# Optimization experiments

Hardware: AMD Instinct MI355X
Metric: run time of the kernel (lower is better)

Reference implementation:

```python
import jax, jax.numpy as jnp
import numpy as np

NUM_FIELDS = 39
PER_FIELD_VOCAB = 10000
TOTAL_VOCAB = NUM_FIELDS * PER_FIELD_VOCAB
EMBED_DIM = 128
DIM_INT = (2, 3)
RANKS = (128, 128)
BATCH = 2048


def setup_inputs() -> dict:
    key = jax.random.key(0)
    k_x, k_emb, k_lin, k_b, k_w0, k_w1 = jax.random.split(key, 6)
    x = jax.random.randint(k_x, (BATCH, NUM_FIELDS), 0, PER_FIELD_VOCAB, dtype=jnp.int64 if jax.config.jax_enable_x64 else jnp.int32)
    embed_table = jax.random.normal(k_emb, (TOTAL_VOCAB, EMBED_DIM), dtype=jnp.float32) * 0.01
    linear_table = jax.random.normal(k_lin, (TOTAL_VOCAB, 1), dtype=jnp.float32) * 0.01
    bias = jnp.zeros((1,), dtype=jnp.float32)
    # trunc_normal_(std=0.01) approximated by scaled normal (same distribution family)
    W0 = jax.random.normal(k_w0, (DIM_INT[0], RANKS[0], NUM_FIELDS), dtype=jnp.float32) * 0.01
    W1 = jax.random.normal(k_w1, (DIM_INT[1], RANKS[1], NUM_FIELDS), dtype=jnp.float32) * 0.01
    return {"x": x, "embed_table": embed_table, "linear_table": linear_table,
            "bias": bias, "W0": W0, "W1": W1}


def _calc_cross(emb, W):
    # emb: [B, F, D]; W: [L, R, F]
    # dot_products[b,d,r,l] = sum_f W[l,r,f] * emb[b,f,d]   (torch: 'bljk,bki->bijl')
    dp = jnp.einsum('lrf,bfd->bdrl', W, emb)          # [B, D, R, L]
    prod_over_l = jnp.prod(dp, axis=3)                # [B, D, R]
    return jnp.sum(prod_over_l, axis=(1, 2))[:, None]  # [B, 1]


def reference(x, embed_table, linear_table, bias, W0, W1):
    # per-field offsets into the flat embedding table (FeaturesEmbedding behavior)
    offsets = (jnp.arange(NUM_FIELDS) * PER_FIELD_VOCAB).astype(x.dtype)
    idx = x + offsets[None, :]                        # [B, F]
    emb = embed_table[idx]                            # [B, F, D]
    # FeaturesLinear: sum of per-feature weights + bias -> [B, 1]
    ret = jnp.sum(linear_table[idx], axis=1) + bias
    for W in (W0, W1):
        ret = ret + _calc_cross(emb, W)
    return (ret, 0)
```

## Files before the change

kernel.cpp:

```cpp
#include <hip/hip_runtime.h>
#include <hip/hip_bf16.h>

#define NUM_FIELDS 39
#define PER_FIELD_VOCAB 10000
#define EMBED_DIM 128
#define KPAD 64
#define NL 5
#define RANK 128
#define BATCH 2048
#define LDS_STRIDE 72

typedef __bf16  bf16x8  __attribute__((ext_vector_type(8)));
typedef float   f32x4   __attribute__((ext_vector_type(4)));

__global__ __launch_bounds__(256) void prep_w(const float* __restrict__ W0,
                                              const float* __restrict__ W1,
                                              __bf16* __restrict__ Wb) {
    int i = blockIdx.x * 256 + threadIdx.x;
    if (i >= NL * RANK * KPAD) return;
    int f = i & (KPAD - 1);
    int r = (i >> 6) & (RANK - 1);
    int l = i >> 13;
    float v = 0.f;
    if (f < NUM_FIELDS) {
        if (l < 2) v = W0[(l * RANK + r) * NUM_FIELDS + f];
        else       v = W1[((l - 2) * RANK + r) * NUM_FIELDS + f];
    }
    Wb[i] = (__bf16)v;
}

__global__ __launch_bounds__(256) void tfm_main(const int* __restrict__ x,
                                                const float* __restrict__ embed_table,
                                                const float* __restrict__ linear_table,
                                                const float* __restrict__ bias,
                                                const __bf16* __restrict__ Wb,
                                                float* __restrict__ out,
                                                int out_size) {
    __shared__ int   sidx[NUM_FIELDS];
    __shared__ __align__(16) __bf16 eT[EMBED_DIM * LDS_STRIDE];
    __shared__ float wpart[4];

    const int tid = threadIdx.x;
    const int b   = blockIdx.x;

    if (tid < NUM_FIELDS)
        sidx[tid] = x[b * NUM_FIELDS + tid] + tid * PER_FIELD_VOCAB;
    __syncthreads();

    for (int k = tid; k < NUM_FIELDS * EMBED_DIM; k += 256) {
        int f = k >> 7, d = k & (EMBED_DIM - 1);
        float v = embed_table[(long)sidx[f] * EMBED_DIM + d];
        eT[d * LDS_STRIDE + f] = (__bf16)v;
    }
    for (int k = tid; k < (KPAD - NUM_FIELDS) * EMBED_DIM; k += 256) {
        int f = NUM_FIELDS + (k >> 7), d = k & (EMBED_DIM - 1);
        eT[d * LDS_STRIDE + f] = (__bf16)0.f;
    }

    float partial = 0.f;
    if (tid < NUM_FIELDS) partial = linear_table[sidx[tid]];

    __syncthreads();

    const int wave = tid >> 6, lane = tid & 63;
    const int m = lane & 15, quad = lane >> 4;

    for (int rti = 0; rti < 2; ++rti) {
        const int r0 = (wave * 2 + rti) * 16;
        bf16x8 afrag[NL][2];
#pragma unroll
        for (int l = 0; l < NL; ++l)
#pragma unroll
            for (int kc = 0; kc < 2; ++kc)
                afrag[l][kc] = *reinterpret_cast<const bf16x8*>(
                    &Wb[((size_t)(l * RANK) + r0 + m) * KPAD + kc * 32 + quad * 8]);

        for (int dt = 0; dt < 8; ++dt) {
            const int d0 = dt * 16;
            bf16x8 bfrag[2];
#pragma unroll
            for (int kc = 0; kc < 2; ++kc)
                bfrag[kc] = *reinterpret_cast<const bf16x8*>(
                    &eT[(d0 + m) * LDS_STRIDE + kc * 32 + quad * 8]);

            f32x4 acc[NL];
#pragma unroll
            for (int l = 0; l < NL; ++l) {
                acc[l] = (f32x4){0.f, 0.f, 0.f, 0.f};
#pragma unroll
                for (int kc = 0; kc < 2; ++kc)
                    acc[l] = __builtin_amdgcn_mfma_f32_16x16x32_bf16(
                        afrag[l][kc], bfrag[kc], acc[l], 0, 0, 0);
            }
#pragma unroll
            for (int i = 0; i < 4; ++i)
                partial += acc[0][i] * acc[1][i] + acc[2][i] * acc[3][i] * acc[4][i];
        }
    }

#pragma unroll
    for (int off = 32; off > 0; off >>= 1)
        partial += __shfl_down(partial, off, 64);
    if (lane == 0) wpart[wave] = partial;
    __syncthreads();
    if (tid == 0)
        out[b] = wpart[0] + wpart[1] + wpart[2] + wpart[3] + bias[0];

    if (b == 0)
        for (int j = BATCH + tid; j < out_size; j += 256)
            out[j] = 0.f;
}

extern "C" void kernel_launch(void* const* d_in, const int* in_sizes, int n_in,
                              void* d_out, int out_size, void* d_ws, size_t ws_size,
                              hipStream_t stream) {
    const int*   x            = (const int*)d_in[0];
    const float* embed_table  = (const float*)d_in[1];
    const float* linear_table = (const float*)d_in[2];
    const float* bias         = (const float*)d_in[3];
    const float* W0           = (const float*)d_in[4];
    const float* W1           = (const float*)d_in[5];
    __bf16*      Wb           = (__bf16*)d_ws;

    prep_w<<<(NL * RANK * KPAD + 255) / 256, 256, 0, stream>>>(W0, W1, Wb);
    tfm_main<<<BATCH, 256, 0, stream>>>(x, embed_table, linear_table, bias, Wb,
                                        (float*)d_out, out_size);
}
```

Baseline: 278.1 us.

## Switch to 32x32x16 MFMA tiles with K padded to 48 and hoisted weight loads

Replaces the 16x16x32 MFMA tiling with 32x32x16 tiles, so each wave handles 32 ranks across all 128 embedding dims. The reduction dimension is padded to 48 instead of 64, which cuts the wasted MFMA work on zero fields. Weight fragments are loaded before the embedding gather so their latency overlaps it. The gather now writes four fields per packed LDS store, with zero padding built in, removing the separate zero-fill loop. The cost is more accumulator registers (five 16-float accumulators plus psum), which may lower occupancy.

```diff
diff --git a/kernel.cpp b/kernel.cpp
--- a/kernel.cpp
+++ b/kernel.cpp
@@ -4,23 +4,25 @@
 #define NUM_FIELDS 39
 #define PER_FIELD_VOCAB 10000
 #define EMBED_DIM 128
-#define KPAD 64
+#define KPAD 48
 #define NL 5
 #define RANK 128
 #define BATCH 2048
-#define LDS_STRIDE 72
+#define LDE 56
 
 typedef __bf16  bf16x8  __attribute__((ext_vector_type(8)));
-typedef float   f32x4   __attribute__((ext_vector_type(4)));
+typedef __bf16  bf16x4  __attribute__((ext_vector_type(4)));
+typedef float   f32x16  __attribute__((ext_vector_type(16)));
 
 __global__ __launch_bounds__(256) void prep_w(const float* __restrict__ W0,
                                               const float* __restrict__ W1,
                                               __bf16* __restrict__ Wb) {
     int i = blockIdx.x * 256 + threadIdx.x;
     if (i >= NL * RANK * KPAD) return;
-    int f = i & (KPAD - 1);
-    int r = (i >> 6) & (RANK - 1);
-    int l = i >> 13;
+    int f  = i % KPAD;
+    int rl = i / KPAD;
+    int r  = rl & (RANK - 1);
+    int l  = rl >> 7;
     float v = 0.f;
     if (f < NUM_FIELDS) {
         if (l < 2) v = W0[(l * RANK + r) * NUM_FIELDS + f];
@@ -37,66 +39,79 @@
                                                 float* __restrict__ out,
                                                 int out_size) {
     __shared__ int   sidx[NUM_FIELDS];
-    __shared__ __align__(16) __bf16 eT[EMBED_DIM * LDS_STRIDE];
+    __shared__ __align__(16) __bf16 eT[EMBED_DIM * LDE];
     __shared__ float wpart[4];
 
-    const int tid = threadIdx.x;
-    const int b   = blockIdx.x;
+    const int tid  = threadIdx.x;
+    const int b    = blockIdx.x;
+    const int wave = tid >> 6, lane = tid & 63;
+    const int ln   = lane & 31, hw = lane >> 5;
 
     if (tid < NUM_FIELDS)
         sidx[tid] = x[b * NUM_FIELDS + tid] + tid * PER_FIELD_VOCAB;
     __syncthreads();
 
-    for (int k = tid; k < NUM_FIELDS * EMBED_DIM; k += 256) {
-        int f = k >> 7, d = k & (EMBED_DIM - 1);
-        float v = embed_table[(long)sidx[f] * EMBED_DIM + d];
-        eT[d * LDS_STRIDE + f] = (__bf16)v;
+    const int rr = wave * 32 + ln;
+    bf16x8 af[NL][3];
+#pragma unroll
+    for (int l = 0; l < NL; ++l)
+#pragma unroll
+        for (int kc = 0; kc < 3; ++kc)
+            af[l][kc] = *reinterpret_cast<const bf16x8*>(
+                &Wb[(size_t)(l * RANK + rr) * KPAD + kc * 16 + hw * 8]);
+
+    float partial = (tid < NUM_FIELDS) ? linear_table[sidx[tid]] : 0.f;
+
+#pragma unroll
+    for (int it = 0; it < 6; ++it) {
+        int u  = it * 256 + tid;
+        int f4 = u >> 7;
+        int d  = u & (EMBED_DIM - 1);
+        int f  = f4 * 4;
+        float v0 = 0.f, v1 = 0.f, v2 = 0.f, v3 = 0.f;
+        if (f + 0 < NUM_FIELDS) v0 = embed_table[(long)sidx[f + 0] * EMBED_DIM + d];
+        if (f + 1 < NUM_FIELDS) v1 = embed_table[(long)sidx[f + 1] * EMBED_DIM + d];
+        if (f + 2 < NUM_FIELDS) v2 = embed_table[(long)sidx[f + 2] * EMBED_DIM + d];
+        if (f + 3 < NUM_FIELDS) v3 = embed_table[(long)sidx[f + 3] * EMBED_DIM + d];
+        bf16x4 pk = {(__bf16)v0, (__bf16)v1, (__bf16)v2, (__bf16)v3};
+        *reinterpret_cast<bf16x4*>(&eT[d * LDE + f4 * 4]) = pk;
     }
-    for (int k = tid; k < (KPAD - NUM_FIELDS) * EMBED_DIM; k += 256) {
-        int f = NUM_FIELDS + (k >> 7), d = k & (EMBED_DIM - 1);
-        eT[d * LDS_STRIDE + f] = (__bf16)0.f;
+    __syncthreads();
+
+    f32x16 zacc;
+#pragma unroll
+    for (int i = 0; i < 16; ++i) zacc[i] = 0.f;
+    f32x16 psum = zacc;
+
+#pragma unroll
+    for (int dt = 0; dt < 4; ++dt) {
+        const __bf16* ep = &eT[(dt * 32 + ln) * LDE + hw * 8];
+        bf16x8 bf0 = *reinterpret_cast<const bf16x8*>(ep);
+        bf16x8 bf1 = *reinterpret_cast<const bf16x8*>(ep + 16);
+        bf16x8 bf2 = *reinterpret_cast<const bf16x8*>(ep + 32);
+
+        f32x16 a0 = __builtin_amdgcn_mfma_f32_32x32x16_bf16(af[0][0], bf0, zacc, 0, 0, 0);
+        a0 = __builtin_amdgcn_mfma_f32_32x32x16_bf16(af[0][1], bf1, a0, 0, 0, 0);
+        a0 = __builtin_amdgcn_mfma_f32_32x32x16_bf16(af[0][2], bf2, a0, 0, 0, 0);
+        f32x16 a1 = __builtin_amdgcn_mfma_f32_32x32x16_bf16(af[1][0], bf0, zacc, 0, 0, 0);
+        a1 = __builtin_amdgcn_mfma_f32_32x32x16_bf16(af[1][1], bf1, a1, 0, 0, 0);
+        a1 = __builtin_amdgcn_mfma_f32_32x32x16_bf16(af[1][2], bf2, a1, 0, 0, 0);
+        f32x16 b0 = __builtin_amdgcn_mfma_f32_32x32x16_bf16(af[2][0], bf0, zacc, 0, 0, 0);
+        b0 = __builtin_amdgcn_mfma_f32_32x32x16_bf16(af[2][1], bf1, b0, 0, 0, 0);
+        b0 = __builtin_amdgcn_mfma_f32_32x32x16_bf16(af[2][2], bf2, b0, 0, 0, 0);
+        f32x16 b1 = __builtin_amdgcn_mfma_f32_32x32x16_bf16(af[3][0], bf0, zacc, 0, 0, 0);
+        b1 = __builtin_amdgcn_mfma_f32_32x32x16_bf16(af[3][1], bf1, b1, 0, 0, 0);
+        b1 = __builtin_amdgcn_mfma_f32_32x32x16_bf16(af[3][2], bf2, b1, 0, 0, 0);
+        f32x16 b2 = __builtin_amdgcn_mfma_f32_32x32x16_bf16(af[4][0], bf0, zacc, 0, 0, 0);
+        b2 = __builtin_amdgcn_mfma_f32_32x32x16_bf16(af[4][1], bf1, b2, 0, 0, 0);
+        b2 = __builtin_amdgcn_mfma_f32_32x32x16_bf16(af[4][2], bf2, b2, 0, 0, 0);
+
+        psum += a0 * a1;
+        psum += b0 * b1 * b2;
     }
 
-    float partial = 0.f;
-    if (tid < NUM_FIELDS) partial = linear_table[sidx[tid]];
-
-    __syncthreads();
-
-    const int wave = tid >> 6, lane = tid & 63;
-    const int m = lane & 15, quad = lane >> 4;
-
-    for (int rti = 0; rti < 2; ++rti) {
-        const int r0 = (wave * 2 + rti) * 16;
-        bf16x8 afrag[NL][2];
 #pragma unroll
-        for (int l = 0; l < NL; ++l)
-#pragma unroll
-            for (int kc = 0; kc < 2; ++kc)
-                afrag[l][kc] = *reinterpret_cast<const bf16x8*>(
-                    &Wb[((size_t)(l * RANK) + r0 + m) * KPAD + kc * 32 + quad * 8]);
-
-        for (int dt = 0; dt < 8; ++dt) {
-            const int d0 = dt * 16;
-            bf16x8 bfrag[2];
-#pragma unroll
-            for (int kc = 0; kc < 2; ++kc)
-                bfrag[kc] = *reinterpret_cast<const bf16x8*>(
-                    &eT[(d0 + m) * LDS_STRIDE + kc * 32 + quad * 8]);
-
-            f32x4 acc[NL];
-#pragma unroll
-            for (int l = 0; l < NL; ++l) {
-                acc[l] = (f32x4){0.f, 0.f, 0.f, 0.f};
-#pragma unroll
-                for (int kc = 0; kc < 2; ++kc)
-                    acc[l] = __builtin_amdgcn_mfma_f32_16x16x32_bf16(
-                        afrag[l][kc], bfrag[kc], acc[l], 0, 0, 0);
-            }
-#pragma unroll
-            for (int i = 0; i < 4; ++i)
-                partial += acc[0][i] * acc[1][i] + acc[2][i] * acc[3][i] * acc[4][i];
-        }
-    }
+    for (int i = 0; i < 16; ++i) partial += psum[i];
 
 #pragma unroll
     for (int off = 32; off > 0; off >>= 1)
```

Measured after the change: 289.5 us. 1.04x slower.

## Use 512 threads with XOR-swizzled LDS and packed 16-byte embedding stores

Applied to the files above, without the earlier changes.

Doubles the block to 8 waves, so each wave handles one 16-row rank tile instead of looping over two. The embedding gather now has each thread load 8 fields for one dimension and write them as a single 16-byte bf16 vector into an XOR-swizzled LDS layout, replacing scalar strided stores and the separate zero-padding loop. Per-lane partial sums are accumulated as a vector and reduced once at the end. The gather now issues 8 dependent-index loads per thread, and the larger block raises register and occupancy pressure.

```diff
diff --git a/kernel.cpp b/kernel.cpp
--- a/kernel.cpp
+++ b/kernel.cpp
@@ -8,7 +8,6 @@
 #define NL 5
 #define RANK 128
 #define BATCH 2048
-#define LDS_STRIDE 72
 
 typedef __bf16  bf16x8  __attribute__((ext_vector_type(8)));
 typedef float   f32x4   __attribute__((ext_vector_type(4)));
@@ -29,7 +28,7 @@
     Wb[i] = (__bf16)v;
 }
 
-__global__ __launch_bounds__(256) void tfm_main(const int* __restrict__ x,
+__global__ __launch_bounds__(512) void tfm_main(const int* __restrict__ x,
                                                 const float* __restrict__ embed_table,
                                                 const float* __restrict__ linear_table,
                                                 const float* __restrict__ bias,
@@ -37,8 +36,8 @@
                                                 float* __restrict__ out,
                                                 int out_size) {
     __shared__ int   sidx[NUM_FIELDS];
-    __shared__ __align__(16) __bf16 eT[EMBED_DIM * LDS_STRIDE];
-    __shared__ float wpart[4];
+    __shared__ __align__(16) __bf16 eT[EMBED_DIM * KPAD];
+    __shared__ float wpart[8];
 
     const int tid = threadIdx.x;
     const int b   = blockIdx.x;
@@ -47,67 +46,80 @@
         sidx[tid] = x[b * NUM_FIELDS + tid] + tid * PER_FIELD_VOCAB;
     __syncthreads();
 
-    for (int k = tid; k < NUM_FIELDS * EMBED_DIM; k += 256) {
-        int f = k >> 7, d = k & (EMBED_DIM - 1);
-        float v = embed_table[(long)sidx[f] * EMBED_DIM + d];
-        eT[d * LDS_STRIDE + f] = (__bf16)v;
+    float partial = (tid < NUM_FIELDS) ? linear_table[sidx[tid]] : 0.f;
+
+    char* eTb = (char*)eT;
+#pragma unroll
+    for (int it = 0; it < 2; ++it) {
+        int u  = it * 512 + tid;
+        int f8 = u >> 7;
+        int d  = u & (EMBED_DIM - 1);
+        float v[8];
+#pragma unroll
+        for (int j = 0; j < 8; ++j) {
+            int f = f8 * 8 + j;
+            v[j] = (f < NUM_FIELDS) ? embed_table[(long)sidx[f] * EMBED_DIM + d]
+                                    : 0.f;
+        }
+        bf16x8 pk;
+#pragma unroll
+        for (int j = 0; j < 8; ++j) pk[j] = (__bf16)v[j];
+        int off = d * 128 + ((f8 * 16) ^ ((d & 7) << 4));
+        *reinterpret_cast<bf16x8*>(eTb + off) = pk;
     }
-    for (int k = tid; k < (KPAD - NUM_FIELDS) * EMBED_DIM; k += 256) {
-        int f = NUM_FIELDS + (k >> 7), d = k & (EMBED_DIM - 1);
-        eT[d * LDS_STRIDE + f] = (__bf16)0.f;
-    }
-
-    float partial = 0.f;
-    if (tid < NUM_FIELDS) partial = linear_table[sidx[tid]];
-
     __syncthreads();
 
     const int wave = tid >> 6, lane = tid & 63;
     const int m = lane & 15, quad = lane >> 4;
+    const int r0 = wave * 16;
 
-    for (int rti = 0; rti < 2; ++rti) {
-        const int r0 = (wave * 2 + rti) * 16;
-        bf16x8 afrag[NL][2];
+    bf16x8 afrag[NL][2];
 #pragma unroll
-        for (int l = 0; l < NL; ++l)
+    for (int l = 0; l < NL; ++l)
+#pragma unroll
+        for (int kc = 0; kc < 2; ++kc)
+            afrag[l][kc] = *reinterpret_cast<const bf16x8*>(
+                &Wb[(size_t)(l * RANK + r0 + m) * KPAD + kc * 32 + quad * 8]);
+
+    f32x4 psum = {0.f, 0.f, 0.f, 0.f};
+
+    for (int dt = 0; dt < 8; ++dt) {
+        const int row = dt * 16 + m;
+        bf16x8 bfrag[2];
+#pragma unroll
+        for (int kc = 0; kc < 2; ++kc) {
+            int off = row * 128 + ((kc * 64 + quad * 16) ^ ((m & 7) << 4));
+            bfrag[kc] = *reinterpret_cast<const bf16x8*>(eTb + off);
+        }
+
+        f32x4 acc[NL];
+#pragma unroll
+        for (int l = 0; l < NL; ++l) {
+            acc[l] = (f32x4){0.f, 0.f, 0.f, 0.f};
 #pragma unroll
             for (int kc = 0; kc < 2; ++kc)
-                afrag[l][kc] = *reinterpret_cast<const bf16x8*>(
-                    &Wb[((size_t)(l * RANK) + r0 + m) * KPAD + kc * 32 + quad * 8]);
+                acc[l] = __builtin_amdgcn_mfma_f32_16x16x32_bf16(
+                    afrag[l][kc], bfrag[kc], acc[l], 0, 0, 0);
+        }
+        psum += acc[0] * acc[1] + acc[2] * acc[3] * acc[4];
+    }
 
-        for (int dt = 0; dt < 8; ++dt) {
-            const int d0 = dt * 16;
-            bf16x8 bfrag[2];
-#pragma unroll
-            for (int kc = 0; kc < 2; ++kc)
-                bfrag[kc] = *reinterpret_cast<const bf16x8*>(
-                    &eT[(d0 + m) * LDS_STRIDE + kc * 32 + quad * 8]);
-
-            f32x4 acc[NL];
-#pragma unroll
-            for (int l = 0; l < NL; ++l) {
-                acc[l] = (f32x4){0.f, 0.f, 0.f, 0.f};
-#pragma unroll
-                for (int kc = 0; kc < 2; ++kc)
-                    acc[l] = __builtin_amdgcn_mfma_f32_16x16x32_bf16(
-                        afrag[l][kc], bfrag[kc], acc[l], 0, 0, 0);
-            }
-#pragma unroll
-            for (int i = 0; i < 4; ++i)
-                partial += acc[0][i] * acc[1][i] + acc[2][i] * acc[3][i] * acc[4][i];
-        }
-    }
+    partial += psum[0] + psum[1] + psum[2] + psum[3];
 
 #pragma unroll
     for (int off = 32; off > 0; off >>= 1)
         partial += __shfl_down(partial, off, 64);
     if (lane == 0) wpart[wave] = partial;
     __syncthreads();
-    if (tid == 0)
-        out[b] = wpart[0] + wpart[1] + wpart[2] + wpart[3] + bias[0];
+    if (tid == 0) {
+        float s = bias[0];
+#pragma unroll
+        for (int w = 0; w < 8; ++w) s += wpart[w];
+        out[b] = s;
+    }
 
     if (b == 0)
-        for (int j = BATCH + tid; j < out_size; j += 256)
+        for (int j = BATCH + tid; j < out_size; j += 512)
             out[j] = 0.f;
 }
 
@@ -123,6 +135,6 @@
     __bf16*      Wb           = (__bf16*)d_ws;
 
     prep_w<<<(NL * RANK * KPAD + 255) / 256, 256, 0, stream>>>(W0, W1, Wb);
-    tfm_main<<<BATCH, 256, 0, stream>>>(x, embed_table, linear_table, bias, Wb,
+    tfm_main<<<BATCH, 512, 0, stream>>>(x, embed_table, linear_table, bias, Wb,
                                         (float*)d_out, out_size);
 }
```

Result: slower. 287.3 us (+3.3%).
